# Kernel tuning notes

Measured on AMD Instinct MI355X. Metric: run time of the kernel, lower is better.

Reference implementation:

```python
import jax, jax.numpy as jnp
import numpy as np

LATENT = 512
CIN = 512
COUT = 512
K = 3
B, H, W = 16, 64, 64

# equalized-lr multipliers (use_wscale=True, lrmul=1, gain=1)
W_MUL_CONV = (CIN * K * K) ** (-0.5)
W_MUL_DENSE = LATENT ** (-0.5)


def setup_inputs() -> dict:
    key = jax.random.key(0)
    k1, k2, k3, k4 = jax.random.split(key, 4)
    x = jax.random.normal(k1, (B, CIN, H, W), dtype=jnp.float32)
    y = jax.random.normal(k2, (B, LATENT), dtype=jnp.float32)
    dense_w = jax.random.normal(k3, (CIN, LATENT), dtype=jnp.float32)
    dense_b = jnp.ones((CIN,), dtype=jnp.float32)  # style bias, init 1 (StyleGAN2)
    weight = jax.random.normal(k4, (COUT, CIN, K, K), dtype=jnp.float32)
    return {"x": x, "y": y, "dense_w": dense_w, "dense_b": dense_b, "weight": weight}


def reference(x, y, dense_w, dense_b, weight):
    # style: s[b, cin] = (y @ dense_w.T) * w_mul + bias (linear bias_act)
    s = jnp.einsum('bl,cl->bc', y, dense_w) * W_MUL_DENSE + dense_b  # [B, Cin]

    # modulate: per-sample weights ww[b,o,i,kh,kw]
    w = weight * W_MUL_CONV
    ww = w[None] * s[:, None, :, None, None]  # [B, Cout, Cin, K, K]

    # demodulate
    d = jax.lax.rsqrt(jnp.sum(ww * ww, axis=(2, 3, 4)) + 1e-8)  # [B, Cout]
    ww = ww * d[:, :, None, None, None]

    # fused grouped conv: groups = B, VALID padding (F.conv2d default)
    b = x.shape[0]
    x_g = x.reshape(1, b * CIN, H, W)
    w_g = ww.reshape(b * COUT, CIN, K, K)
    out = jax.lax.conv_general_dilated(
        x_g, w_g,
        window_strides=(1, 1), padding='VALID',
        dimension_numbers=('NCHW', 'OIHW', 'NCHW'),
        feature_group_count=b)
    return out.reshape(b, COUT, H - K + 1, W - K + 1)
```

## Files before the change

### kernel.cpp

```cpp
#include <hip/hip_runtime.h>
#include <hip/hip_bf16.h>

#define CIN 512
#define COUT 512
#define BATCH 16
#define NP 3844
#define OW 62

#define W_MUL_DENSE 0.044194173824159216f
#define W_MUL_CONV  0.014731391274719736f

using short8  = __attribute__((ext_vector_type(8))) short;
using floatx4 = __attribute__((ext_vector_type(4))) float;
using uintx4  = __attribute__((ext_vector_type(4))) unsigned int;

__device__ __forceinline__ unsigned short f2bfu(float f) {
    unsigned u = __builtin_bit_cast(unsigned, f);
    u += 0x7FFFu + ((u >> 16) & 1u);
    return (unsigned short)(u >> 16);
}

__device__ __forceinline__ void gload_lds16(const void* g, void* l) {
    __builtin_amdgcn_global_load_lds(
        (const __attribute__((address_space(1))) void*)g,
        (__attribute__((address_space(3))) void*)l, 16, 0, 0);
}


__global__ void emc_style_kernel(const float* __restrict__ y, const float* __restrict__ dw,
                                 const float* __restrict__ db, float* __restrict__ s) {
    int idx = blockIdx.x * 256 + threadIdx.x;
    int b = idx >> 9, c = idx & 511;
    const float4* yb = (const float4*)(y + b * 512);
    const float4* wc = (const float4*)(dw + c * 512);
    float acc = 0.f;
#pragma unroll 4
    for (int l = 0; l < 128; ++l) {
        float4 a = yb[l], w4 = wc[l];
        acc += a.x * w4.x + a.y * w4.y + a.z * w4.z + a.w * w4.w;
    }
    s[idx] = acc * W_MUL_DENSE + db[c];
}

__global__ void emc_wsq_kernel(const float* __restrict__ w, float* __restrict__ wsq) {
    int idx = blockIdx.x * 256 + threadIdx.x;
    const float* p = w + (size_t)idx * 9;
    float a = 0.f;
#pragma unroll
    for (int j = 0; j < 9; ++j) a += p[j] * p[j];
    wsq[idx] = a;
}

__global__ void emc_demod_kernel(const float* __restrict__ s, const float* __restrict__ wsq,
                                 float* __restrict__ d) {
    int idx = blockIdx.x * 256 + threadIdx.x;
    int b = idx >> 9, o = idx & 511;
    const float4* sb = (const float4*)(s + b * 512);
    const float4* wo = (const float4*)(wsq + o * 512);
    float acc = 0.f;
#pragma unroll 4
    for (int l = 0; l < 128; ++l) {
        float4 a = sb[l], c = wo[l];
        acc += a.x * a.x * c.x + a.y * a.y * c.y + a.z * a.z * c.z + a.w * a.w * c.w;
    }
    d[idx] = rsqrtf(W_MUL_CONV * W_MUL_CONV * acc + 1e-8f);
}

__global__ void emc_wrepack_kernel(const float* __restrict__ w, unsigned short* __restrict__ wb) {
    int idx = blockIdx.x * 256 + threadIdx.x;
    int i = idx & 511;
    int r = idx >> 9;
    int kpos = r % 9;
    int o = r / 9;
    wb[idx] = f2bfu(w[(size_t)(o * 512 + i) * 9 + kpos]);
}


__global__ __launch_bounds__(256, 2) void emc_conv_kernel(
    const float* __restrict__ x, const unsigned short* __restrict__ wb,
    const float* __restrict__ sv, const float* __restrict__ dv,
    float* __restrict__ out) {

    __shared__ __align__(16) unsigned short smA[3][256 * 32];
    __shared__ __align__(16) unsigned short smB[260 * 40];
    __shared__ float s_s[512];
    __shared__ float s_d[256];

    int orig = blockIdx.x;
    int cpx = gridDim.x >> 3;
    int bid = (orig & 7) * cpx + (orig >> 3);

    int b = bid / 62;
    int t = bid - b * 62;
    int ot = t & 1;
    int strip = t >> 1;
    int oB = ot * 256;
    int r0 = strip * 2;

    int tid = threadIdx.x;
    int lane = tid & 63;
    int wid = tid >> 6;

    s_s[tid]       = sv[b * 512 + tid];
    s_s[tid + 256] = sv[b * 512 + 256 + tid];
    s_d[tid]       = dv[b * 512 + oB + tid];

    int sc = tid & 63;
    int sr = tid >> 6;
    const float* xrow = x + (size_t)b * (512 * 4096) + (r0 + sr) * 64 + sc;
    unsigned short* bg = smB + (sr * 64 + sc) * 40;

    const unsigned short* asrc[4];
    int adst[4];
#pragma unroll
    for (int j = 0; j < 4; ++j) {
        int row = wid * 64 + j * 16 + (lane >> 2);
        asrc[j] = wb + (size_t)(oB + row) * 4608 + (((lane & 3) ^ ((row >> 1) & 3)) << 3);
        adst[j] = (wid * 64 + j * 16) * 32;
    }

    int frc = lane & 15, q = lane >> 4;
    int wr = wid >> 1, wc = wid & 1;
    int aidx[8], bidx[4];
#pragma unroll
    for (int m = 0; m < 8; ++m) {
        int row = wr * 128 + m * 16 + frc;
        aidx[m] = row * 32 + ((q ^ ((row >> 1) & 3)) << 3);
    }
#pragma unroll
    for (int n = 0; n < 4; ++n) bidx[n] = (wc * 64 + n * 16 + frc) * 40 + q * 8;

    floatx4 acc[8][4];
#pragma unroll
    for (int m = 0; m < 8; ++m)
#pragma unroll
        for (int n = 0; n < 4; ++n) acc[m][n] = floatx4{0.f, 0.f, 0.f, 0.f};

    float raw[8];
    unsigned held[16];

    auto ISSUE_A = [&](int kN, int iN, int bufsel) {
        int off = kN * 512 + iN * 32;
#pragma unroll
        for (int j = 0; j < 4; ++j)
            gload_lds16(asrc[j] + off, &smA[bufsel][adst[j]]);
    };

    auto LOAD_SLICE = [&](int itgt, int sl) {
        const float* xp = xrow + ((size_t)itgt * 32 + sl * 4) * 4096;
        int r = (sl & 1) * 4;
        raw[r + 0] = xp[0];
        raw[r + 1] = xp[4096];
        raw[r + 2] = xp[2 * 4096];
        raw[r + 3] = xp[3 * 4096];
    };

    auto CONVERT = [&](int itgt, int sl) {
        int i0 = itgt * 32 + sl * 4;
        int r = (sl & 1) * 4;
        float v0 = raw[r + 0] * s_s[i0];
        float v1 = raw[r + 1] * s_s[i0 + 1];
        float v2 = raw[r + 2] * s_s[i0 + 2];
        float v3 = raw[r + 3] * s_s[i0 + 3];
        held[2 * sl]     = (unsigned)f2bfu(v0) | ((unsigned)f2bfu(v1) << 16);
        held[2 * sl + 1] = (unsigned)f2bfu(v2) | ((unsigned)f2bfu(v3) << 16);
    };

    auto WRITE_B = [&]() {
        *(uintx4*)(bg)      = uintx4{held[0],  held[1],  held[2],  held[3]};
        *(uintx4*)(bg + 8)  = uintx4{held[4],  held[5],  held[6],  held[7]};
        *(uintx4*)(bg + 16) = uintx4{held[8],  held[9],  held[10], held[11]};
        *(uintx4*)(bg + 24) = uintx4{held[12], held[13], held[14], held[15]};
    };

    auto COMPUTE = [&](int kpos, int bufsel) {
        int kh = kpos / 3, kw = kpos - kh * 3;
        int bo = (kh * 64 + kw) * 40;
        const unsigned short* A = smA[bufsel];
        short8 bfr[4];
#pragma unroll
        for (int n = 0; n < 4; ++n) bfr[n] = *(const short8*)(smB + bidx[n] + bo);
        __builtin_amdgcn_s_setprio(1);
#pragma unroll
        for (int mh = 0; mh < 2; ++mh) {
            short8 af[4];
#pragma unroll
            for (int mm = 0; mm < 4; ++mm) af[mm] = *(const short8*)(A + aidx[mh * 4 + mm]);
#pragma unroll
            for (int mm = 0; mm < 4; ++mm)
#pragma unroll
                for (int n = 0; n < 4; ++n)
                    acc[mh * 4 + mm][n] = __builtin_amdgcn_mfma_f32_16x16x32_bf16(
                        af[mm], bfr[n], acc[mh * 4 + mm][n], 0, 0, 0);
        }
        __builtin_amdgcn_s_setprio(0);
    };

    __syncthreads();

    ISSUE_A(0, 0, 0);
    ISSUE_A(1, 0, 1);
#pragma unroll
    for (int sl = 0; sl < 8; ++sl) {
        LOAD_SLICE(0, sl);
        if (sl > 0) CONVERT(0, sl - 1);
    }
    CONVERT(0, 7);
    WRITE_B();
    asm volatile("s_waitcnt lgkmcnt(0)" ::: "memory");
    __builtin_amdgcn_s_barrier();

    for (int itile = 0; itile < 15; ++itile) {
#pragma unroll
        for (int kpos = 0; kpos < 9; ++kpos) {
            {
                int kN = (kpos + 2) % 9;
                int iN = itile + (kpos + 2) / 9;
                ISSUE_A(kN, iN, (kpos + 2) % 3);
            }
            if (kpos < 8) LOAD_SLICE(itile + 1, kpos);
            if (kpos >= 1) CONVERT(itile + 1, kpos - 1);
            COMPUTE(kpos, kpos % 3);
            if (kpos == 8) {
                __builtin_amdgcn_s_barrier();
                WRITE_B();
                asm volatile("s_waitcnt lgkmcnt(0)" ::: "memory");
                __builtin_amdgcn_s_barrier();
            } else {
                asm volatile("s_waitcnt vmcnt(8)" ::: "memory");
                __builtin_amdgcn_s_barrier();
            }
        }
    }

#pragma unroll
    for (int kpos = 0; kpos < 9; ++kpos) {
        if (kpos <= 6) {
            int kN = (kpos + 2) % 9;
            ISSUE_A(kN, 15, (kpos + 2) % 3);
        }
        COMPUTE(kpos, kpos % 3);
        if (kpos < 7) {
            asm volatile("s_waitcnt vmcnt(4)" ::: "memory");
            __builtin_amdgcn_s_barrier();
        } else if (kpos == 7) {
            asm volatile("s_waitcnt vmcnt(0)" ::: "memory");
            __builtin_amdgcn_s_barrier();
        }
    }

    size_t outb = (size_t)b * 512 * NP;
#pragma unroll
    for (int m = 0; m < 8; ++m) {
#pragma unroll
        for (int r = 0; r < 4; ++r) {
            int o_l = wr * 128 + m * 16 + q * 4 + r;
            float scale = W_MUL_CONV * s_d[o_l];
            size_t rb = outb + (size_t)(oB + o_l) * NP + strip * 124 + wc * OW;
#pragma unroll
            for (int n = 0; n < 4; ++n) {
                int col = n * 16 + frc;
                if (col < OW) out[rb + col] = acc[m][n][r] * scale;
            }
        }
    }
}

extern "C" void kernel_launch(void* const* d_in, const int* in_sizes, int n_in,
                              void* d_out, int out_size, void* d_ws, size_t ws_size,
                              hipStream_t stream) {
    const float* x  = (const float*)d_in[0];
    const float* y  = (const float*)d_in[1];
    const float* dw = (const float*)d_in[2];
    const float* db = (const float*)d_in[3];
    const float* w  = (const float*)d_in[4];
    float* out = (float*)d_out;

    char* ws = (char*)d_ws;
    float* s_  = (float*)ws;
    float* d_  = (float*)(ws + 32768);
    float* wsq = (float*)(ws + 65536);
    unsigned short* wb = (unsigned short*)(ws + 65536 + 1048576);

    emc_style_kernel<<<32, 256, 0, stream>>>(y, dw, db, s_);
    emc_wsq_kernel<<<1024, 256, 0, stream>>>(w, wsq);
    emc_demod_kernel<<<32, 256, 0, stream>>>(s_, wsq, d_);
    emc_wrepack_kernel<<<9216, 256, 0, stream>>>(w, wb);
    emc_conv_kernel<<<16 * 62, 256, 0, stream>>>(x, wb, s_, d_, out);
}
```

Before: 350.7 us.

## Load weight fragments directly into registers instead of staging through LDS

Removes the triple-buffered LDS staging of the bf16 weight tile (global_load_lds). Each wave now loads its own 64-row A fragments straight from global memory into registers, double-buffered two kernel positions ahead. The wave layout changes from a 2x2 split to each wave owning 64 output channels across all 128 pixels, and the per-kpos barriers are dropped. This cuts LDS usage and synchronisation, but it relies on per-lane global loads hiding latency without the barrier-based pipeline. It also leans on the compiler to insert correct waitcnts for the register-resident loads.

```diff
diff --git a/kernel.cpp b/kernel.cpp
--- a/kernel.cpp
+++ b/kernel.cpp
@@ -18,12 +18,6 @@
     unsigned u = __builtin_bit_cast(unsigned, f);
     u += 0x7FFFu + ((u >> 16) & 1u);
     return (unsigned short)(u >> 16);
-}
-
-__device__ __forceinline__ void gload_lds16(const void* g, void* l) {
-    __builtin_amdgcn_global_load_lds(
-        (const __attribute__((address_space(1))) void*)g,
-        (__attribute__((address_space(3))) void*)l, 16, 0, 0);
 }
 
 
@@ -81,7 +75,6 @@
     const float* __restrict__ sv, const float* __restrict__ dv,
     float* __restrict__ out) {
 
-    __shared__ __align__(16) unsigned short smA[3][256 * 32];
     __shared__ __align__(16) unsigned short smB[260 * 40];
     __shared__ float s_s[512];
     __shared__ float s_d[256];
@@ -110,40 +103,34 @@
     const float* xrow = x + (size_t)b * (512 * 4096) + (r0 + sr) * 64 + sc;
     unsigned short* bg = smB + (sr * 64 + sc) * 40;
 
-    const unsigned short* asrc[4];
-    int adst[4];
-#pragma unroll
-    for (int j = 0; j < 4; ++j) {
-        int row = wid * 64 + j * 16 + (lane >> 2);
-        asrc[j] = wb + (size_t)(oB + row) * 4608 + (((lane & 3) ^ ((row >> 1) & 3)) << 3);
-        adst[j] = (wid * 64 + j * 16) * 32;
-    }
-
     int frc = lane & 15, q = lane >> 4;
-    int wr = wid >> 1, wc = wid & 1;
-    int aidx[8], bidx[4];
-#pragma unroll
-    for (int m = 0; m < 8; ++m) {
-        int row = wr * 128 + m * 16 + frc;
-        aidx[m] = row * 32 + ((q ^ ((row >> 1) & 3)) << 3);
-    }
-#pragma unroll
-    for (int n = 0; n < 4; ++n) bidx[n] = (wc * 64 + n * 16 + frc) * 40 + q * 8;
-
-    floatx4 acc[8][4];
-#pragma unroll
-    for (int m = 0; m < 8; ++m)
-#pragma unroll
-        for (int n = 0; n < 4; ++n) acc[m][n] = floatx4{0.f, 0.f, 0.f, 0.f};
-
+
+    int voffA[4];
+#pragma unroll
+    for (int m = 0; m < 4; ++m)
+        voffA[m] = (wid * 64 + m * 16 + frc) * 9216 + q * 16;
+
+    int bidx[8];
+#pragma unroll
+    for (int n = 0; n < 8; ++n) bidx[n] = (n * 16 + frc) * 40 + q * 8;
+
+    floatx4 acc[4][8];
+#pragma unroll
+    for (int m = 0; m < 4; ++m)
+#pragma unroll
+        for (int n = 0; n < 8; ++n) acc[m][n] = floatx4{0.f, 0.f, 0.f, 0.f};
+
+    short8 fA0[4], fA1[4];
     float raw[8];
     unsigned held[16];
 
-    auto ISSUE_A = [&](int kN, int iN, int bufsel) {
-        int off = kN * 512 + iN * 32;
-#pragma unroll
-        for (int j = 0; j < 4; ++j)
-            gload_lds16(asrc[j] + off, &smA[bufsel][adst[j]]);
+    const char* wbB = (const char*)wb + (size_t)oB * 9216;
+
+    auto AISSUE = [&](int it, int kN, short8* dst) {
+        const char* abase = wbB + (kN * 512 + it * 32) * 2;
+#pragma unroll
+        for (int m = 0; m < 4; ++m)
+            dst[m] = *(const short8*)(abase + voffA[m]);
     };
 
     auto LOAD_SLICE = [&](int itgt, int sl) {
@@ -173,33 +160,44 @@
         *(uintx4*)(bg + 24) = uintx4{held[12], held[13], held[14], held[15]};
     };
 
-    auto COMPUTE = [&](int kpos, int bufsel) {
+    auto MFMA32 = [&](int kpos, short8* fc) {
         int kh = kpos / 3, kw = kpos - kh * 3;
         int bo = (kh * 64 + kw) * 40;
-        const unsigned short* A = smA[bufsel];
-        short8 bfr[4];
-#pragma unroll
-        for (int n = 0; n < 4; ++n) bfr[n] = *(const short8*)(smB + bidx[n] + bo);
+        short8 bfr[8];
+#pragma unroll
+        for (int n = 0; n < 8; ++n) bfr[n] = *(const short8*)(smB + bidx[n] + bo);
         __builtin_amdgcn_s_setprio(1);
 #pragma unroll
-        for (int mh = 0; mh < 2; ++mh) {
-            short8 af[4];
-#pragma unroll
-            for (int mm = 0; mm < 4; ++mm) af[mm] = *(const short8*)(A + aidx[mh * 4 + mm]);
-#pragma unroll
-            for (int mm = 0; mm < 4; ++mm)
-#pragma unroll
-                for (int n = 0; n < 4; ++n)
-                    acc[mh * 4 + mm][n] = __builtin_amdgcn_mfma_f32_16x16x32_bf16(
-                        af[mm], bfr[n], acc[mh * 4 + mm][n], 0, 0, 0);
+        for (int m = 0; m < 4; ++m)
+#pragma unroll
+            for (int n = 0; n < 8; ++n)
+                acc[m][n] = __builtin_amdgcn_mfma_f32_16x16x32_bf16(
+                    fc[m], bfr[n], acc[m][n], 0, 0, 0);
+        __builtin_amdgcn_s_setprio(0);
+    };
+
+    auto PHASE = [&](int it, int kpos, int par, bool stage, bool issueNext) {
+        short8* fc = par ? fA1 : fA0;
+        if (stage && kpos < 8) LOAD_SLICE(it + 1, kpos);
+        if (stage && kpos >= 1) CONVERT(it + 1, kpos - 1);
+        MFMA32(kpos, fc);
+        if (issueNext) {
+            int iN = (kpos >= 7) ? it + 1 : it;
+            int kN = (kpos + 2) % 9;
+            AISSUE(iN, kN, fc);
         }
-        __builtin_amdgcn_s_setprio(0);
+        if (stage && kpos == 8) {
+            __builtin_amdgcn_s_barrier();
+            WRITE_B();
+            asm volatile("s_waitcnt lgkmcnt(0)" ::: "memory");
+            __builtin_amdgcn_s_barrier();
+        }
     };
 
     __syncthreads();
 
-    ISSUE_A(0, 0, 0);
-    ISSUE_A(1, 0, 1);
+    AISSUE(0, 0, fA0);
+    AISSUE(0, 1, fA1);
 #pragma unroll
     for (int sl = 0; sl < 8; ++sl) {
         LOAD_SLICE(0, sl);
@@ -207,60 +205,33 @@
     }
     CONVERT(0, 7);
     WRITE_B();
-    asm volatile("s_waitcnt lgkmcnt(0)" ::: "memory");
-    __builtin_amdgcn_s_barrier();
-
-    for (int itile = 0; itile < 15; ++itile) {
-#pragma unroll
-        for (int kpos = 0; kpos < 9; ++kpos) {
-            {
-                int kN = (kpos + 2) % 9;
-                int iN = itile + (kpos + 2) / 9;
-                ISSUE_A(kN, iN, (kpos + 2) % 3);
-            }
-            if (kpos < 8) LOAD_SLICE(itile + 1, kpos);
-            if (kpos >= 1) CONVERT(itile + 1, kpos - 1);
-            COMPUTE(kpos, kpos % 3);
-            if (kpos == 8) {
-                __builtin_amdgcn_s_barrier();
-                WRITE_B();
-                asm volatile("s_waitcnt lgkmcnt(0)" ::: "memory");
-                __builtin_amdgcn_s_barrier();
-            } else {
-                asm volatile("s_waitcnt vmcnt(8)" ::: "memory");
-                __builtin_amdgcn_s_barrier();
-            }
-        }
-    }
-
-#pragma unroll
-    for (int kpos = 0; kpos < 9; ++kpos) {
-        if (kpos <= 6) {
-            int kN = (kpos + 2) % 9;
-            ISSUE_A(kN, 15, (kpos + 2) % 3);
-        }
-        COMPUTE(kpos, kpos % 3);
-        if (kpos < 7) {
-            asm volatile("s_waitcnt vmcnt(4)" ::: "memory");
-            __builtin_amdgcn_s_barrier();
-        } else if (kpos == 7) {
-            asm volatile("s_waitcnt vmcnt(0)" ::: "memory");
-            __builtin_amdgcn_s_barrier();
-        }
-    }
+    __syncthreads();
+
+    for (int itp = 0; itp < 7; ++itp) {
+        int ite = itp * 2, ito = itp * 2 + 1;
+#pragma unroll
+        for (int k = 0; k < 9; ++k) PHASE(ite, k, k & 1, true, true);
+#pragma unroll
+        for (int k = 0; k < 9; ++k) PHASE(ito, k, (k + 1) & 1, true, true);
+    }
+#pragma unroll
+    for (int k = 0; k < 9; ++k) PHASE(14, k, k & 1, true, true);
+#pragma unroll
+    for (int k = 0; k < 9; ++k) PHASE(15, k, (k + 1) & 1, false, k <= 6);
 
     size_t outb = (size_t)b * 512 * NP;
 #pragma unroll
-    for (int m = 0; m < 8; ++m) {
+    for (int m = 0; m < 4; ++m) {
 #pragma unroll
         for (int r = 0; r < 4; ++r) {
-            int o_l = wr * 128 + m * 16 + q * 4 + r;
+            int o_l = wid * 64 + m * 16 + q * 4 + r;
             float scale = W_MUL_CONV * s_d[o_l];
-            size_t rb = outb + (size_t)(oB + o_l) * NP + strip * 124 + wc * OW;
-#pragma unroll
-            for (int n = 0; n < 4; ++n) {
-                int col = n * 16 + frc;
-                if (col < OW) out[rb + col] = acc[m][n][r] * scale;
+            size_t rb = outb + (size_t)(oB + o_l) * NP + strip * 124;
+#pragma unroll
+            for (int n = 0; n < 8; ++n) {
+                int row = n >> 2;
+                int col = (n & 3) * 16 + frc;
+                if (col < OW) out[rb + row * OW + col] = acc[m][n][r] * scale;
             }
         }
     }
```

Result: slower. 384.0 us (+9.5%).
